# Kernel optimization log

Measured on AMD Instinct MI355X. Metric: run time of the kernel, lower is better.

Reference implementation:

```python
import jax, jax.numpy as jnp
import numpy as np

N, F_IN, HID, HEADS, NCLS, E = 50000, 512, 64, 4, 64, 800000
NEG_SLOPE = 0.2
EPS = 1e-16


def setup_inputs() -> dict:
    key = jax.random.key(0)
    ks = jax.random.split(key, 10)
    s = 0.1
    return {
        "x": jax.random.normal(ks[0], (N, F_IN), jnp.float32),
        "edge_index": jax.random.randint(ks[1], (2, E), 0, N, jnp.int64),
        "W1": jax.random.normal(ks[2], (F_IN, HEADS * HID), jnp.float32) * s,
        "a_src1": jax.random.normal(ks[3], (HEADS, HID), jnp.float32) * s,
        "a_dst1": jax.random.normal(ks[4], (HEADS, HID), jnp.float32) * s,
        "b1": jax.random.normal(ks[5], (HEADS * HID,), jnp.float32) * s,
        "W2": jax.random.normal(ks[6], (HEADS * HID, NCLS), jnp.float32) * s,
        "a_src2": jax.random.normal(ks[7], (1, NCLS), jnp.float32) * s,
        "a_dst2": jax.random.normal(ks[8], (1, NCLS), jnp.float32) * s,
        "b2": jax.random.normal(ks[9], (NCLS,), jnp.float32) * s,
    }


def gat_conv(x, W, a_src, a_dst, b, src, dst):
    H, C = a_src.shape
    h = (x @ W).reshape(-1, H, C)                     # [N, H, C]
    # per-node attention halves, gathered per edge -> [E', H]
    al_src = jnp.einsum("nhc,hc->nh", h, a_src)
    al_dst = jnp.einsum("nhc,hc->nh", h, a_dst)
    e = jax.nn.leaky_relu(al_src[src] + al_dst[dst], NEG_SLOPE)
    # segment softmax over destination neighborhoods
    m = jax.ops.segment_max(e, dst, num_segments=x.shape[0])
    ex = jnp.exp(e - m[dst])
    denom = jax.ops.segment_sum(ex, dst, num_segments=x.shape[0])
    alpha = ex / (denom[dst] + EPS)                   # [E', H]
    out = jax.ops.segment_sum(alpha[:, :, None] * h[src], dst,
                              num_segments=x.shape[0])  # [N, H, C]
    return out.reshape(-1, H * C) + b


def reference(x, edge_index, W1, a_src1, a_dst1, b1, W2, a_src2, a_dst2, b2):
    n = x.shape[0]
    loop = jnp.arange(n, dtype=edge_index.dtype)
    src = jnp.concatenate([edge_index[0], loop])       # add self loops (PyG default)
    dst = jnp.concatenate([edge_index[1], loop])
    h = gat_conv(x, W1, a_src1, a_dst1, b1, src, dst)
    h = jax.nn.elu(h)                                  # dropout is identity in eval
    out = gat_conv(h, W2, a_src2, a_dst2, b2, src, dst)
    return jax.nn.log_softmax(out, axis=1)
```

## Files before the change

### kernel.cpp

```cpp
#include <hip/hip_runtime.h>
#include <math.h>

#define F_IN 512
#define HC1 256
#define HEADS 4
#define HID 64
#define NCLS 64
#define NEG_SLOPE 0.2f
#define EPS_DENOM 1e-16f

using short8 = __attribute__((ext_vector_type(8))) short;
using f32x4  = __attribute__((ext_vector_type(4))) float;

__device__ inline float wave_sum(float v) {
#pragma unroll
  for (int s = 32; s > 0; s >>= 1) v += __shfl_xor(v, s);
  return v;
}

__device__ inline unsigned short f2bf(float f) {
  unsigned int u = __float_as_uint(f);
  u = (u + 0x7FFF + ((u >> 16) & 1)) >> 16;
  return (unsigned short)u;
}
__device__ inline float bflo(unsigned int u) { return __uint_as_float(u << 16); }
__device__ inline float bfhi(unsigned int u) { return __uint_as_float(u & 0xFFFF0000u); }

__device__ inline unsigned int cvtpk_bf16(float lo, float hi) {
  unsigned int r;
  asm("v_cvt_pk_bf16_f32 %0, %1, %2" : "=v"(r) : "v"(lo), "v"(hi));
  return r;
}

__device__ inline void async_copy16(const void* g, void* l) {
  __builtin_amdgcn_global_load_lds((const __attribute__((address_space(1))) void*)g,
                                   (__attribute__((address_space(3))) void*)l, 16, 0, 0);
}

__global__ void castT_kernel(const float* __restrict__ W, unsigned short* __restrict__ WT,
                             int K, int Nn) {
  int id = blockIdx.x * blockDim.x + threadIdx.x;
  if (id >= K * Nn) return;
  int n = id / K, k = id % K;
  WT[id] = f2bf(W[(size_t)k * Nn + n]);
}


__global__ void hist_kernel(const int* __restrict__ dst, int E, int* __restrict__ cnt) {
  int i = blockIdx.x * blockDim.x + threadIdx.x;
  int stride = gridDim.x * blockDim.x;
  for (int e = i; e < E; e += stride) atomicAdd(&cnt[dst[e]], 1);
}

__global__ void scan_blocks_kernel(const int* __restrict__ cnt, int n,
                                   int* __restrict__ rowoff, int* __restrict__ cursor,
                                   int* __restrict__ bsum) {
  __shared__ int wpart[16];
  int b = blockIdx.x, tid = threadIdx.x;
  int i = b * 1024 + tid;
  int lane = tid & 63, wid = tid >> 6;
  int v = (i < n) ? (cnt[i] + 1) : 0;
  int x = v;
#pragma unroll
  for (int s = 1; s < 64; s <<= 1) {
    int t = __shfl_up(x, s);
    if (lane >= s) x += t;
  }
  if (lane == 63) wpart[wid] = x;
  __syncthreads();
  if (wid == 0) {
    int p = (lane < 16) ? wpart[lane] : 0;
#pragma unroll
    for (int s = 1; s < 16; s <<= 1) {
      int t = __shfl_up(p, s);
      if (lane >= s) p += t;
    }
    if (lane < 16) wpart[lane] = p;
  }
  __syncthreads();
  int incl = x + (wid ? wpart[wid - 1] : 0);
  if (i < n) { rowoff[i + 1] = incl; cursor[i] = incl - v; }
  if (tid == 1023) bsum[b] = incl;
  if (b == 0 && tid == 0) rowoff[0] = 0;
}

__global__ void scan_partials_kernel(int* __restrict__ bsum, int nb) {
  int lane = threadIdx.x;
  int v = (lane < nb) ? bsum[lane] : 0;
  int x = v;
#pragma unroll
  for (int s = 1; s < 64; s <<= 1) {
    int t = __shfl_up(x, s);
    if (lane >= s) x += t;
  }
  if (lane < nb) bsum[lane] = x - v;
}

__global__ void scan_add_kernel(int n, int* __restrict__ rowoff, int* __restrict__ cursor,
                                const int* __restrict__ bsum) {
  int i = blockIdx.x * 1024 + threadIdx.x;
  int off = bsum[blockIdx.x];
  if (i < n) { rowoff[i + 1] += off; cursor[i] += off; }
}

__global__ void scatter_kernel(const int* __restrict__ src, const int* __restrict__ dst,
                               int E, int n, int* __restrict__ cursor, int* __restrict__ esrc) {
  int i = blockIdx.x * blockDim.x + threadIdx.x;
  int stride = gridDim.x * blockDim.x;
  for (int e = i; e < E + n; e += stride) {
    int s, d;
    if (e < E) { s = src[e]; d = dst[e]; } else { s = e - E; d = s; }
    int pos = atomicAdd(&cursor[d], 1);
    esrc[pos] = s;
  }
}


__global__ __launch_bounds__(512)
void gemm1_fused_kernel(const float* __restrict__ A, const unsigned short* __restrict__ BT,
                        unsigned short* __restrict__ Cb,
                        const float* __restrict__ as1, const float* __restrict__ ad1,
                        float* __restrict__ als, float* __restrict__ ald, int M) {
  constexpr int BM = 128, BN = 256, BK = 32, K = F_IN, Nn = HC1;
  __shared__ unsigned short Alds[2][BM * BK];
  __shared__ unsigned short Blds[2][BN * BK];
  const int t = threadIdx.x;
  const int lane = t & 63;
  const int w = t >> 6;
  const int wr = (w >> 2) * 64;
  const int wc = (w & 3) * 64;
  const int head = w & 3;
  const int row0 = blockIdx.x * BM;
  const int lrow = lane & 15;
  const int lk = (lane >> 4) * 8;

  f32x4 acc[4][4] = {};

  const int ar = t >> 2, kq = (t & 3) * 8;
  int grow = row0 + ar; if (grow > M - 1) grow = M - 1;
  const float* aptr = A + (size_t)grow * K + kq;

  float4 fa0, fa1;
  fa0 = *(const float4*)(aptr);
  fa1 = *(const float4*)(aptr + 4);
#pragma unroll
  for (int i = 0; i < 2; ++i) {
    int c = i * 512 + t;
    const unsigned short* g = BT + (size_t)(c >> 2) * K + (c & 3) * 8;
    async_copy16(g, &Blds[0][(size_t)c * 8]);
  }
  {
    uint4 u;
    u.x = cvtpk_bf16(fa0.x, fa0.y); u.y = cvtpk_bf16(fa0.z, fa0.w);
    u.z = cvtpk_bf16(fa1.x, fa1.y); u.w = cvtpk_bf16(fa1.z, fa1.w);
    *(uint4*)&Alds[0][ar * BK + kq] = u;
  }
  int cur = 0;
  for (int k0 = 0; k0 < K; k0 += BK) {
    __syncthreads();
    const int nxt = cur ^ 1;
    const bool more = (k0 + BK) < K;
    if (more) {
#pragma unroll
      for (int i = 0; i < 2; ++i) {
        int c = i * 512 + t;
        const unsigned short* g = BT + (size_t)(c >> 2) * K + (k0 + BK) + (c & 3) * 8;
        async_copy16(g, &Blds[nxt][(size_t)c * 8]);
      }
      fa0 = *(const float4*)(aptr + k0 + BK);
      fa1 = *(const float4*)(aptr + k0 + BK + 4);
    }
    short8 a[4], b[4];
#pragma unroll
    for (int m = 0; m < 4; ++m)
      a[m] = *(const short8*)&Alds[cur][(wr + m * 16 + lrow) * BK + lk];
#pragma unroll
    for (int n = 0; n < 4; ++n)
      b[n] = *(const short8*)&Blds[cur][(wc + n * 16 + lrow) * BK + lk];
#pragma unroll
    for (int m = 0; m < 4; ++m)
#pragma unroll
      for (int n = 0; n < 4; ++n)
        acc[m][n] = __builtin_amdgcn_mfma_f32_16x16x32_bf16(a[m], b[n], acc[m][n], 0, 0, 0);
    if (more) {
      uint4 u;
      u.x = cvtpk_bf16(fa0.x, fa0.y); u.y = cvtpk_bf16(fa0.z, fa0.w);
      u.z = cvtpk_bf16(fa1.x, fa1.y); u.w = cvtpk_bf16(fa1.z, fa1.w);
      *(uint4*)&Alds[nxt][ar * BK + kq] = u;
    }
    cur = nxt;
  }

  float asv[4], adv[4];
#pragma unroll
  for (int n = 0; n < 4; ++n) {
    asv[n] = as1[head * 64 + n * 16 + lrow];
    adv[n] = ad1[head * 64 + n * 16 + lrow];
  }
#pragma unroll
  for (int m = 0; m < 4; ++m) {
#pragma unroll
    for (int j = 0; j < 4; ++j) {
      int r = row0 + wr + m * 16 + (lane >> 4) * 4 + j;
      float ps = 0.f, pd = 0.f;
#pragma unroll
      for (int n = 0; n < 4; ++n) {
        float v = acc[m][n][j];
        ps += v * asv[n];
        pd += v * adv[n];
        if (r < M) Cb[(size_t)r * Nn + wc + n * 16 + lrow] = f2bf(v);
      }
#pragma unroll
      for (int s = 1; s < 16; s <<= 1) {
        ps += __shfl_xor(ps, s);
        pd += __shfl_xor(pd, s);
      }
      if ((lane & 15) == 0 && r < M) {
        als[r * HEADS + head] = ps;
        ald[r * HEADS + head] = pd;
      }
    }
  }
}


__global__ __launch_bounds__(256)
void gemm2_fused_kernel(const unsigned short* __restrict__ A,
                        const unsigned short* __restrict__ BT,
                        unsigned short* __restrict__ Cb,
                        const float* __restrict__ as2, const float* __restrict__ ad2,
                        float* __restrict__ als, float* __restrict__ ald, int M) {
  constexpr int BM = 128, BN = 64, BK = 32, K = HC1, Nn = NCLS;
  __shared__ unsigned short Alds[BM * BK];
  __shared__ unsigned short Blds[BN * BK];
  __shared__ float sps[BM], spd[BM];
  const int t = threadIdx.x;
  const int lane = t & 63;
  const int w = t >> 6;
  const int wr = (w >> 1) * 64;
  const int wc = (w & 1) * 32;
  const int row0 = blockIdx.x * BM;
  const int lrow = lane & 15;
  const int lk = (lane >> 4) * 8;
  if (t < BM) { sps[t] = 0.f; spd[t] = 0.f; }

  f32x4 acc[4][2] = {};
  for (int k0 = 0; k0 < K; k0 += BK) {
#pragma unroll
    for (int i = 0; i < 2; ++i) {
      int c = i * 256 + t;
      int arr = c >> 2;
      int ak = (c & 3) * 8;
      int grow = row0 + arr; if (grow > M - 1) grow = M - 1;
      const unsigned short* g = A + (size_t)grow * K + k0 + ak;
      unsigned short* l = Alds + (size_t)(i * 256 + w * 64) * 8;
      async_copy16(g, l);
    }
    {
      int c = t;
      int br = c >> 2;
      int bk = (c & 3) * 8;
      const unsigned short* g = BT + (size_t)br * K + k0 + bk;
      unsigned short* l = Blds + (size_t)(w * 64) * 8;
      async_copy16(g, l);
    }
    __syncthreads();
    short8 a[4], b[2];
#pragma unroll
    for (int m = 0; m < 4; ++m)
      a[m] = *(const short8*)&Alds[(wr + m * 16 + lrow) * BK + lk];
#pragma unroll
    for (int n = 0; n < 2; ++n)
      b[n] = *(const short8*)&Blds[(wc + n * 16 + lrow) * BK + lk];
#pragma unroll
    for (int m = 0; m < 4; ++m)
#pragma unroll
      for (int n = 0; n < 2; ++n)
        acc[m][n] = __builtin_amdgcn_mfma_f32_16x16x32_bf16(a[m], b[n], acc[m][n], 0, 0, 0);
    __syncthreads();
  }

  float asv[2], adv[2];
#pragma unroll
  for (int n = 0; n < 2; ++n) {
    asv[n] = as2[wc + n * 16 + lrow];
    adv[n] = ad2[wc + n * 16 + lrow];
  }
#pragma unroll
  for (int m = 0; m < 4; ++m) {
#pragma unroll
    for (int j = 0; j < 4; ++j) {
      int rl = wr + m * 16 + (lane >> 4) * 4 + j;
      int r = row0 + rl;
      float ps = 0.f, pd = 0.f;
#pragma unroll
      for (int n = 0; n < 2; ++n) {
        float v = acc[m][n][j];
        ps += v * asv[n];
        pd += v * adv[n];
        if (r < M) Cb[(size_t)r * Nn + wc + n * 16 + lrow] = f2bf(v);
      }
#pragma unroll
      for (int s = 1; s < 16; s <<= 1) {
        ps += __shfl_xor(ps, s);
        pd += __shfl_xor(pd, s);
      }
      if ((lane & 15) == 0) {
        atomicAdd(&sps[rl], ps);
        atomicAdd(&spd[rl], pd);
      }
    }
  }
  __syncthreads();
  if (t < BM) {
    int r = row0 + t;
    if (r < M) { als[r] = sps[t]; ald[r] = spd[t]; }
  }
}


__global__ void agg1_kernel(const unsigned short* __restrict__ h1b,
                            const float4* __restrict__ als1, const float4* __restrict__ ald1,
                            const int* __restrict__ rowoff, const int* __restrict__ esrc,
                            const float* __restrict__ b1, unsigned short* __restrict__ hact,
                            int n) {
  __shared__ float wlds[4][256];
  __shared__ int   slds[4][64];
  int w = threadIdx.x >> 6;
  int node = blockIdx.x * 4 + w;
  if (node >= n) return;
  int lane = threadIdx.x & 63;
  int hi = lane >> 5;
  int cl = lane & 31;
  int head = cl >> 3;
  int beg = rowoff[node], end = rowoff[node + 1];
  float4 aldn = ald1[node];
  f32x4 accA = {0.f, 0.f, 0.f, 0.f};
  f32x4 accB = {0.f, 0.f, 0.f, 0.f};
  float dl0 = 0.f, dl1 = 0.f, dl2 = 0.f, dl3 = 0.f;

  for (int base = beg; base < end; base += 64) {
    int cnt = min(64, end - base);
    if (lane < cnt) {
      int s = esrc[base + lane];
      float4 av = als1[s];
      float v, w0, w1, w2, w3;
      v = av.x + aldn.x; v = fmaxf(v, NEG_SLOPE * v); w0 = __expf(v);
      v = av.y + aldn.y; v = fmaxf(v, NEG_SLOPE * v); w1 = __expf(v);
      v = av.z + aldn.z; v = fmaxf(v, NEG_SLOPE * v); w2 = __expf(v);
      v = av.w + aldn.w; v = fmaxf(v, NEG_SLOPE * v); w3 = __expf(v);
      dl0 += w0; dl1 += w1; dl2 += w2; dl3 += w3;
      slds[w][lane] = s;
      float4 wv = {w0, w1, w2, w3};
      *(float4*)&wlds[w][lane * 4] = wv;
    }

    uint4 dA[4], dB[4];
    float wA[4], wB[4];
    auto ISSUE = [&](int j0, uint4* d, float* wj) {
#pragma unroll
      for (int ii = 0; ii < 4; ++ii) {
        int e = j0 + 2 * ii + hi;
        bool val = e < cnt;
        int se = val ? e : 0;
        int ss = slds[w][se];
        wj[ii] = val ? wlds[w][se * 4 + head] : 0.f;
        d[ii] = *(const uint4*)&h1b[(size_t)ss * HC1 + cl * 8];
      }
    };
    auto CONSUME = [&](const uint4* d, const float* wj) {
#pragma unroll
      for (int ii = 0; ii < 4; ++ii) {
        float q = wj[ii];
        accA[0] += q * bflo(d[ii].x); accA[1] += q * bfhi(d[ii].x);
        accA[2] += q * bflo(d[ii].y); accA[3] += q * bfhi(d[ii].y);
        accB[0] += q * bflo(d[ii].z); accB[1] += q * bfhi(d[ii].z);
        accB[2] += q * bflo(d[ii].w); accB[3] += q * bfhi(d[ii].w);
      }
    };

    ISSUE(0, dA, wA);
    for (int j0 = 8;; j0 += 16) {
      bool hasB = j0 < cnt;
      if (hasB) ISSUE(j0, dB, wB);
      CONSUME(dA, wA);
      if (!hasB) break;
      bool hasA = (j0 + 8) < cnt;
      if (hasA) ISSUE(j0 + 8, dA, wA);
      CONSUME(dB, wB);
      if (!hasA) break;
    }
  }

#pragma unroll
  for (int k = 0; k < 4; ++k) {
    accA[k] += __shfl_xor(accA[k], 32);
    accB[k] += __shfl_xor(accB[k], 32);
  }
  float d0 = wave_sum(dl0), d1 = wave_sum(dl1);
  float d2 = wave_sum(dl2), d3 = wave_sum(dl3);
  float den = head < 2 ? (head == 0 ? d0 : d1) : (head == 2 ? d2 : d3);
  float rden = 1.f / (den + EPS_DENOM);
  if (hi == 0) {
    float4 bv0 = *(const float4*)&b1[cl * 8];
    float4 bv1 = *(const float4*)&b1[cl * 8 + 4];
    float o[8];
    o[0] = accA[0] * rden + bv0.x; o[1] = accA[1] * rden + bv0.y;
    o[2] = accA[2] * rden + bv0.z; o[3] = accA[3] * rden + bv0.w;
    o[4] = accB[0] * rden + bv1.x; o[5] = accB[1] * rden + bv1.y;
    o[6] = accB[2] * rden + bv1.z; o[7] = accB[3] * rden + bv1.w;
    ushort4 ov0, ov1;
#pragma unroll
    for (int k = 0; k < 8; ++k) o[k] = o[k] > 0.f ? o[k] : __expf(o[k]) - 1.f;
    ov0.x = f2bf(o[0]); ov0.y = f2bf(o[1]); ov0.z = f2bf(o[2]); ov0.w = f2bf(o[3]);
    ov1.x = f2bf(o[4]); ov1.y = f2bf(o[5]); ov1.z = f2bf(o[6]); ov1.w = f2bf(o[7]);
    *(ushort4*)&hact[(size_t)node * HC1 + cl * 8] = ov0;
    *(ushort4*)&hact[(size_t)node * HC1 + cl * 8 + 4] = ov1;
  }
}

__global__ void agg2_kernel(const unsigned short* __restrict__ h2b,
                            const float* __restrict__ als2, const float* __restrict__ ald2,
                            const int* __restrict__ rowoff, const int* __restrict__ esrc,
                            const float* __restrict__ b2, float* __restrict__ out, int n) {
  __shared__ float wlds[4][64];
  __shared__ int   slds[4][64];
  int w = threadIdx.x >> 6;
  int node = blockIdx.x * 4 + w;
  if (node >= n) return;
  int lane = threadIdx.x & 63;
  int eg = lane >> 3;
  int cl = lane & 7;
  int beg = rowoff[node], end = rowoff[node + 1];
  float aldn = ald2[node];
  f32x4 accA = {0.f, 0.f, 0.f, 0.f};
  f32x4 accB = {0.f, 0.f, 0.f, 0.f};
  float dl = 0.f;
  for (int base = beg; base < end; base += 64) {
    int cnt = min(64, end - base);
    if (lane < cnt) {
      int s = esrc[base + lane];
      float v = als2[s] + aldn;
      v = fmaxf(v, NEG_SLOPE * v);
      float wl = __expf(v);
      dl += wl;
      slds[w][lane] = s;
      wlds[w][lane] = wl;
    }
    for (int j0 = 0; j0 < cnt; j0 += 32) {
      uint4 d[4]; float wj[4];
#pragma unroll
      for (int ii = 0; ii < 4; ++ii) {
        int e = j0 + ii * 8 + eg;
        bool val = e < cnt;
        int se = val ? e : 0;
        int ss = slds[w][se];
        wj[ii] = val ? wlds[w][se] : 0.f;
        d[ii] = *(const uint4*)&h2b[(size_t)ss * NCLS + cl * 8];
      }
#pragma unroll
      for (int ii = 0; ii < 4; ++ii) {
        float q = wj[ii];
        accA[0] += q * bflo(d[ii].x); accA[1] += q * bfhi(d[ii].x);
        accA[2] += q * bflo(d[ii].y); accA[3] += q * bfhi(d[ii].y);
        accB[0] += q * bflo(d[ii].z); accB[1] += q * bfhi(d[ii].z);
        accB[2] += q * bflo(d[ii].w); accB[3] += q * bfhi(d[ii].w);
      }
    }
  }
#pragma unroll
  for (int s = 8; s < 64; s <<= 1) {
#pragma unroll
    for (int k = 0; k < 4; ++k) {
      accA[k] += __shfl_xor(accA[k], s);
      accB[k] += __shfl_xor(accB[k], s);
    }
  }
  float den = wave_sum(dl);
  float rden = 1.f / (den + EPS_DENOM);
  float4 bv0 = *(const float4*)&b2[cl * 8];
  float4 bv1 = *(const float4*)&b2[cl * 8 + 4];
  float o[8];
  o[0] = accA[0] * rden + bv0.x; o[1] = accA[1] * rden + bv0.y;
  o[2] = accA[2] * rden + bv0.z; o[3] = accA[3] * rden + bv0.w;
  o[4] = accB[0] * rden + bv1.x; o[5] = accB[1] * rden + bv1.y;
  o[6] = accB[2] * rden + bv1.z; o[7] = accB[3] * rden + bv1.w;
  float mx = o[0];
#pragma unroll
  for (int k = 1; k < 8; ++k) mx = fmaxf(mx, o[k]);
#pragma unroll
  for (int s = 1; s < 8; s <<= 1) mx = fmaxf(mx, __shfl_xor(mx, s));
  float sm = 0.f;
#pragma unroll
  for (int k = 0; k < 8; ++k) sm += __expf(o[k] - mx);
#pragma unroll
  for (int s = 1; s < 8; s <<= 1) sm += __shfl_xor(sm, s);
  float ls = mx + __logf(sm);
  if (lane < 8) {
    float4 q0 = {o[0] - ls, o[1] - ls, o[2] - ls, o[3] - ls};
    float4 q1 = {o[4] - ls, o[5] - ls, o[6] - ls, o[7] - ls};
    *(float4*)&out[(size_t)node * NCLS + cl * 8] = q0;
    *(float4*)&out[(size_t)node * NCLS + cl * 8 + 4] = q1;
  }
}


extern "C" void kernel_launch(void* const* d_in, const int* in_sizes, int n_in,
                              void* d_out, int out_size, void* d_ws, size_t ws_size,
                              hipStream_t stream) {
  const float* x      = (const float*)d_in[0];
  const int*   eidx   = (const int*)d_in[1];
  const float* W1     = (const float*)d_in[2];
  const float* a_src1 = (const float*)d_in[3];
  const float* a_dst1 = (const float*)d_in[4];
  const float* b1     = (const float*)d_in[5];
  const float* W2     = (const float*)d_in[6];
  const float* a_src2 = (const float*)d_in[7];
  const float* a_dst2 = (const float*)d_in[8];
  const float* b2     = (const float*)d_in[9];
  float* out = (float*)d_out;

  const int Nn = in_sizes[0] / F_IN;
  const int E  = in_sizes[1] / 2;
  const int* esrc_in = eidx;
  const int* edst_in = eidx + E;

  char* ws = (char*)d_ws;
  size_t off = 0;
  auto alloc = [&](size_t bytes) -> void* {
    void* p = ws + off;
    off += (bytes + 255) & ~(size_t)255;
    return p;
  };
  unsigned short* h1b    = (unsigned short*)alloc((size_t)Nn * HC1 * sizeof(short));
  unsigned short* hact   = (unsigned short*)alloc((size_t)Nn * HC1 * sizeof(short));
  unsigned short* h2b    = (unsigned short*)alloc((size_t)Nn * NCLS * sizeof(short));
  unsigned short* W1T    = (unsigned short*)alloc((size_t)F_IN * HC1 * sizeof(short));
  unsigned short* W2T    = (unsigned short*)alloc((size_t)HC1 * NCLS * sizeof(short));
  float*          als1   = (float*)alloc((size_t)Nn * HEADS * sizeof(float));
  float*          ald1   = (float*)alloc((size_t)Nn * HEADS * sizeof(float));
  float*          als2   = (float*)alloc((size_t)Nn * sizeof(float));
  float*          ald2   = (float*)alloc((size_t)Nn * sizeof(float));
  int*            cnt    = (int*)alloc((size_t)Nn * sizeof(int));
  int*            rowoff = (int*)alloc((size_t)(Nn + 1) * sizeof(int));
  int*            cursor = (int*)alloc((size_t)Nn * sizeof(int));
  int*            bsum   = (int*)alloc(256 * sizeof(int));
  int*            esrc   = (int*)alloc((size_t)(E + Nn) * sizeof(int));

  const int nscan = (Nn + 1023) / 1024;

  castT_kernel<<<(F_IN * HC1 + 255) / 256, 256, 0, stream>>>(W1, W1T, F_IN, HC1);
  castT_kernel<<<(HC1 * NCLS + 255) / 256, 256, 0, stream>>>(W2, W2T, HC1, NCLS);

  hipMemsetAsync(cnt, 0, (size_t)Nn * sizeof(int), stream);
  hist_kernel<<<(E + 255) / 256, 256, 0, stream>>>(edst_in, E, cnt);
  scan_blocks_kernel<<<nscan, 1024, 0, stream>>>(cnt, Nn, rowoff, cursor, bsum);
  scan_partials_kernel<<<1, 64, 0, stream>>>(bsum, nscan);
  scan_add_kernel<<<nscan, 1024, 0, stream>>>(Nn, rowoff, cursor, bsum);
  scatter_kernel<<<(E + Nn + 255) / 256, 256, 0, stream>>>(esrc_in, edst_in, E, Nn, cursor, esrc);

  {
    int blocks = (Nn + 127) / 128;
    gemm1_fused_kernel<<<blocks, 512, 0, stream>>>(x, W1T, h1b, a_src1, a_dst1,
                                                   als1, ald1, Nn);
    int ablocks = (Nn + 3) / 4;
    agg1_kernel<<<ablocks, 256, 0, stream>>>(h1b, (const float4*)als1, (const float4*)ald1,
                                             rowoff, esrc, b1, hact, Nn);
  }

  {
    int blocks = (Nn + 127) / 128;
    gemm2_fused_kernel<<<blocks, 256, 0, stream>>>(hact, W2T, h2b, a_src2, a_dst2,
                                                   als2, ald2, Nn);
    int ablocks = (Nn + 3) / 4;
    agg2_kernel<<<ablocks, 256, 0, stream>>>(h2b, als2, ald2, rowoff, esrc, b2, out, Nn);
  }
}
```

Before: 261.4 us.

## Stage fp32 A tiles via async copies with XOR-swizzled LDS in gemm1

Reworks the first GEMM so both the fp32 activation tile and the bf16 weight tile are loaded into LDS with async 16-byte copies using XOR-swizzled layouts. The bf16 conversion now happens at LDS read time instead of through registers before the LDS write. The block tile shrinks to 64 rows with 256 threads, each wave taking one head's 64 columns. The aim is to overlap global loads with MFMA work, avoid LDS bank conflicts, and raise block count and occupancy. In exchange, LDS traffic for A doubles because it is stored as fp32, and each block reuses the B tile across fewer rows.

Measured after the change: 266.5 us. No clear change (+2.0%).

```diff
diff --git a/kernel.cpp b/kernel.cpp
--- a/kernel.cpp
+++ b/kernel.cpp
@@ -116,92 +116,87 @@
 }
 
 
-__global__ __launch_bounds__(512)
+__global__ __launch_bounds__(256)
 void gemm1_fused_kernel(const float* __restrict__ A, const unsigned short* __restrict__ BT,
                         unsigned short* __restrict__ Cb,
                         const float* __restrict__ as1, const float* __restrict__ ad1,
                         float* __restrict__ als, float* __restrict__ ald, int M) {
-  constexpr int BM = 128, BN = 256, BK = 32, K = F_IN, Nn = HC1;
-  __shared__ unsigned short Alds[2][BM * BK];
-  __shared__ unsigned short Blds[2][BN * BK];
+  constexpr int BM = 64, BN = 256, BK = 32, K = F_IN, Nn = HC1;
+  __shared__ float          Af[2][BM * BK];
+  __shared__ unsigned short Bh[2][BN * BK];
   const int t = threadIdx.x;
   const int lane = t & 63;
   const int w = t >> 6;
-  const int wr = (w >> 2) * 64;
-  const int wc = (w & 3) * 64;
-  const int head = w & 3;
+  const int wc = w * 64;
   const int row0 = blockIdx.x * BM;
   const int lrow = lane & 15;
-  const int lk = (lane >> 4) * 8;
+  const int lkf = (lane >> 4) * 8;
+
+  auto stageA = [&](int buf, int k0) {
+#pragma unroll
+    for (int i = 0; i < 2; ++i) {
+      int c = i * 256 + t;
+      int r = c >> 3, slot = c & 7;
+      int grow = row0 + r; if (grow > M - 1) grow = M - 1;
+      const float* g = A + (size_t)grow * K + k0 + ((slot ^ (r & 7)) << 2);
+      async_copy16(g, (char*)&Af[buf][0] + (size_t)(i * 256 + w * 64) * 16);
+    }
+  };
+  auto stageB = [&](int buf, int k0) {
+#pragma unroll
+    for (int i = 0; i < 4; ++i) {
+      int c = i * 256 + t;
+      int r = c >> 2, slot = c & 3;
+      const unsigned short* g = BT + (size_t)r * K + k0 + ((slot ^ (r & 3)) << 3);
+      async_copy16(g, (char*)&Bh[buf][0] + (size_t)(i * 256 + w * 64) * 16);
+    }
+  };
 
   f32x4 acc[4][4] = {};
-
-  const int ar = t >> 2, kq = (t & 3) * 8;
-  int grow = row0 + ar; if (grow > M - 1) grow = M - 1;
-  const float* aptr = A + (size_t)grow * K + kq;
-
-  float4 fa0, fa1;
-  fa0 = *(const float4*)(aptr);
-  fa1 = *(const float4*)(aptr + 4);
-#pragma unroll
-  for (int i = 0; i < 2; ++i) {
-    int c = i * 512 + t;
-    const unsigned short* g = BT + (size_t)(c >> 2) * K + (c & 3) * 8;
-    async_copy16(g, &Blds[0][(size_t)c * 8]);
-  }
-  {
-    uint4 u;
-    u.x = cvtpk_bf16(fa0.x, fa0.y); u.y = cvtpk_bf16(fa0.z, fa0.w);
-    u.z = cvtpk_bf16(fa1.x, fa1.y); u.w = cvtpk_bf16(fa1.z, fa1.w);
-    *(uint4*)&Alds[0][ar * BK + kq] = u;
-  }
+  stageA(0, 0); stageB(0, 0);
   int cur = 0;
   for (int k0 = 0; k0 < K; k0 += BK) {
     __syncthreads();
-    const int nxt = cur ^ 1;
-    const bool more = (k0 + BK) < K;
-    if (more) {
-#pragma unroll
-      for (int i = 0; i < 2; ++i) {
-        int c = i * 512 + t;
-        const unsigned short* g = BT + (size_t)(c >> 2) * K + (k0 + BK) + (c & 3) * 8;
-        async_copy16(g, &Blds[nxt][(size_t)c * 8]);
-      }
-      fa0 = *(const float4*)(aptr + k0 + BK);
-      fa1 = *(const float4*)(aptr + k0 + BK + 4);
-    }
+    if (k0 + BK < K) { stageA(cur ^ 1, k0 + BK); stageB(cur ^ 1, k0 + BK); }
     short8 a[4], b[4];
 #pragma unroll
-    for (int m = 0; m < 4; ++m)
-      a[m] = *(const short8*)&Alds[cur][(wr + m * 16 + lrow) * BK + lk];
-#pragma unroll
-    for (int n = 0; n < 4; ++n)
-      b[n] = *(const short8*)&Blds[cur][(wc + n * 16 + lrow) * BK + lk];
+    for (int m = 0; m < 4; ++m) {
+      int r = m * 16 + lrow;
+      int s0 = lkf >> 2;
+      const char* base = (const char*)&Af[cur][0] + (size_t)r * 128;
+      float4 f0 = *(const float4*)(base + (((s0    ) ^ (r & 7)) << 4));
+      float4 f1 = *(const float4*)(base + (((s0 | 1) ^ (r & 7)) << 4));
+      union { short8 s; uint4 u; } pk;
+      pk.u.x = cvtpk_bf16(f0.x, f0.y); pk.u.y = cvtpk_bf16(f0.z, f0.w);
+      pk.u.z = cvtpk_bf16(f1.x, f1.y); pk.u.w = cvtpk_bf16(f1.z, f1.w);
+      a[m] = pk.s;
+    }
+#pragma unroll
+    for (int n = 0; n < 4; ++n) {
+      int r = wc + n * 16 + lrow;
+      int slot = lkf >> 3;
+      b[n] = *(const short8*)((const char*)&Bh[cur][0] + (size_t)r * 64 +
+                              (((slot ^ (r & 3))) << 4));
+    }
 #pragma unroll
     for (int m = 0; m < 4; ++m)
 #pragma unroll
       for (int n = 0; n < 4; ++n)
         acc[m][n] = __builtin_amdgcn_mfma_f32_16x16x32_bf16(a[m], b[n], acc[m][n], 0, 0, 0);
-    if (more) {
-      uint4 u;
-      u.x = cvtpk_bf16(fa0.x, fa0.y); u.y = cvtpk_bf16(fa0.z, fa0.w);
-      u.z = cvtpk_bf16(fa1.x, fa1.y); u.w = cvtpk_bf16(fa1.z, fa1.w);
-      *(uint4*)&Alds[nxt][ar * BK + kq] = u;
-    }
-    cur = nxt;
+    cur ^= 1;
   }
 
   float asv[4], adv[4];
 #pragma unroll
   for (int n = 0; n < 4; ++n) {
-    asv[n] = as1[head * 64 + n * 16 + lrow];
-    adv[n] = ad1[head * 64 + n * 16 + lrow];
+    asv[n] = as1[w * 64 + n * 16 + lrow];
+    adv[n] = ad1[w * 64 + n * 16 + lrow];
   }
 #pragma unroll
   for (int m = 0; m < 4; ++m) {
 #pragma unroll
     for (int j = 0; j < 4; ++j) {
-      int r = row0 + wr + m * 16 + (lane >> 4) * 4 + j;
+      int r = row0 + m * 16 + (lane >> 4) * 4 + j;
       float ps = 0.f, pd = 0.f;
 #pragma unroll
       for (int n = 0; n < 4; ++n) {
@@ -216,8 +211,8 @@
         pd += __shfl_xor(pd, s);
       }
       if ((lane & 15) == 0 && r < M) {
-        als[r * HEADS + head] = ps;
-        ald[r * HEADS + head] = pd;
+        als[r * HEADS + w] = ps;
+        ald[r * HEADS + w] = pd;
       }
     }
   }
@@ -560,8 +555,8 @@
   scatter_kernel<<<(E + Nn + 255) / 256, 256, 0, stream>>>(esrc_in, edst_in, E, Nn, cursor, esrc);
 
   {
-    int blocks = (Nn + 127) / 128;
-    gemm1_fused_kernel<<<blocks, 512, 0, stream>>>(x, W1T, h1b, a_src1, a_dst1,
+    int blocks = (Nn + 63) / 64;
+    gemm1_fused_kernel<<<blocks, 256, 0, stream>>>(x, W1T, h1b, a_src1, a_dst1,
                                                    als1, ald1, Nn);
     int ablocks = (Nn + 3) / 4;
     agg1_kernel<<<ablocks, 256, 0, stream>>>(h1b, (const float4*)als1, (const float4*)ald1,
```
